# Kernel tuning notes

Measured on AMD Instinct MI355X. Metric: run time of the kernel, lower is better.

Reference implementation:

```python
import jax, jax.numpy as jnp
import numpy as np

B = 262144
K = 128  # n_coarse == num_bins


def setup_inputs() -> dict:
    key = jax.random.key(0)
    k1, k2, k3, k4, k5 = jax.random.split(key, 5)
    rays = jax.random.normal(k1, (B, 8), dtype=jnp.float32)
    weights = jax.random.uniform(k2, (B, K), dtype=jnp.float32)
    # z_samp must be monotonically increasing depths along each ray (near..far)
    near, far = 0.5, 10.0
    z_raw = jax.random.uniform(k3, (B, K), dtype=jnp.float32)
    z_samp = near + jnp.sort(z_raw, axis=-1) * (far - near)
    u = jax.random.uniform(k4, (B, K), dtype=jnp.float32)
    interval_interp = jax.random.uniform(k5, (B, K), dtype=jnp.float32)
    return {"rays": rays, "weights": weights, "z_samp": z_samp,
            "u": u, "interval_interp": interval_interp}


def reference(rays, weights, z_samp, u, interval_interp):
    # NeRFRenderer.sample_coarse_from_dist (lindisp=False)
    n_samples = u.shape[-1]  # n_coarse
    w = jax.lax.stop_gradient(weights) + 1e-5          # weights.detach() + 1e-5
    pdf = w / jnp.sum(w, axis=-1, keepdims=True)       # (B, K)
    cdf = jnp.cumsum(pdf, axis=-1)
    cdf = jnp.concatenate([jnp.zeros_like(cdf[:, :1]), cdf], axis=-1)  # (B, K+1)
    # searchsorted(cdf, u, right=True) - 1, batched over rays
    interval_ids = jax.vmap(lambda c, uu: jnp.searchsorted(c, uu, side='right'))(cdf, u) - 1
    interval_ids = jnp.clip(interval_ids, 0, n_samples - 1)
    # interval borders: [z0, midpoints, z_{K-1}] -> (B, K+1)
    centers = 0.5 * (z_samp[:, 1:] + z_samp[:, :-1])
    borders = jnp.concatenate([z_samp[:, :1], centers, z_samp[:, -1:]], axis=-1)
    left = jnp.take_along_axis(borders, interval_ids, axis=-1)
    right = jnp.take_along_axis(borders, interval_ids + 1, axis=-1)
    z_new = left * (1.0 - interval_interp) + right * interval_interp
    return z_new
```

## Files before the change

### kernel.cpp

```cpp
#include <hip/hip_runtime.h>

#define KK  128
#define RPW 8
#define TPB 128

__global__ __launch_bounds__(TPB, 6)
void nerf_sample_kernel(const float* __restrict__ Wg,
                        const float* __restrict__ Zg,
                        const float* __restrict__ Ug,
                        const float* __restrict__ Tg,
                        float* __restrict__ Og)
{
    __shared__ float S[2 * 2080];
    const int lane = threadIdx.x & 63;
    const int wvid = threadIdx.x >> 6;
    float* CW = S + wvid * 2080;
    float* BW = CW + 1024;

    const int r   = lane >> 3;
    const int h   = lane & 7;
    const int swz = r << 3;
    float* Srow = CW + r * KK;
    float* Brow = BW + r * 132;

    const size_t grp   = (size_t)blockIdx.x * 2 + wvid;
    const size_t gbase = grp * (RPW * KK);
    const size_t rbase = gbase + (size_t)r * KK;

    float4 cu = *(const float4*)(Ug + gbase + 4 * lane);
    float4 ct = *(const float4*)(Tg + gbase + 4 * lane);

    float x[16];
    {
        const float* wp = Wg + rbase + 16 * h;
        #pragma unroll
        for (int e = 0; e < 4; ++e) {
            float4 v = *(const float4*)(wp + 4 * e);
            x[4*e+0] = v.x + 1e-5f;
            x[4*e+1] = v.y + 1e-5f;
            x[4*e+2] = v.z + 1e-5f;
            x[4*e+3] = v.w + 1e-5f;
        }
    }

    float zr[16];
    {
        const float* zp = Zg + rbase + 16 * h;
        #pragma unroll
        for (int e = 0; e < 4; ++e) {
            float4 v = *(const float4*)(zp + 4 * e);
            zr[4*e+0] = v.x; zr[4*e+1] = v.y; zr[4*e+2] = v.z; zr[4*e+3] = v.w;
        }
    }

    float tot;
    {
        float Cc[16];
        #pragma unroll
        for (int c = 0; c < 16; ++c) {
            float a = x[c] + __shfl_xor(x[c], 4);
            float b = a    + __shfl_xor(a, 1);
            Cc[c]   = b    + __shfl_xor(b, 2);
        }
        float Uu[8];
        #pragma unroll
        for (int c = 0; c < 8; ++c) Uu[c] = Cc[c] + Cc[c + 8];
        float Vv[4];
        #pragma unroll
        for (int c = 0; c < 4; ++c) Vv[c] = Uu[c] + Uu[c + 4];
        tot = (Vv[0] + Vv[2]) + (Vv[1] + Vv[3]);
    }

    #pragma unroll
    for (int j = 0; j < 16; ++j) x[j] = x[j] / tot;

    #pragma unroll
    for (int m = 0; m < 8; ++m) x[2*m+1] = x[2*m+1] + x[2*m];
    #pragma unroll
    for (int m = 0; m < 4; ++m) x[4*m+3] = x[4*m+3] + x[4*m+1];
    #pragma unroll
    for (int m = 0; m < 2; ++m) x[8*m+7] = x[8*m+7] + x[8*m+3];
    x[15] = x[15] + x[7];

    {
        float s    = x[15];
        float sx1  = __shfl_xor(s, 1);
        float t1   = s + sx1;
        float t1x2 = __shfl_xor(t1, 2);
        float t2   = t1 + t1x2;
        float t2x4 = __shfl_xor(t2, 4);
        float c95  = t1x2 + t2x4;

        float xf =
            (h == 0) ? s :
            (h == 1) ? t1 :
            (h == 2) ? s + t1x2 :
            (h == 3) ? t2 :
            (h == 4) ? s + t2x4 :
            (h == 5) ? t1 + t2x4 :
            (h == 6) ? s + c95 :
                       t2 + t2x4;
        x[15] = xf;

        float P =
            (h == 0) ? 0.0f :
            (h == 1) ? sx1 :
            (h == 2) ? t1x2 :
            (h == 3) ? sx1 + t1x2 :
            (h == 4) ? t2x4 :
            (h == 5) ? sx1 + t2x4 :
            (h == 6) ? c95 :
                       sx1 + c95;

        x[7]  = x[7]  + P;
        x[3]  = x[3]  + P;  x[11] = x[11] + x[7];
        x[1]  = x[1]  + P;  x[5]  = x[5]  + x[3];
        x[9]  = x[9]  + x[7];  x[13] = x[13] + x[11];
        x[0]  = x[0]  + P;
        #pragma unroll
        for (int m = 1; m < 8; ++m) x[2*m] = x[2*m] + x[2*m-1];
    }

    #pragma unroll
    for (int e = 0; e < 4; ++e)
        *(float4*)(Srow + ((16*h + 4*e) ^ swz)) =
            make_float4(x[4*e+0], x[4*e+1], x[4*e+2], x[4*e+3]);

    {
        float zprev = __shfl_up(zr[15], 1);
        float B[16];
        B[0] = (h == 0) ? zr[0] : 0.5f * (zr[0] + zprev);
        #pragma unroll
        for (int k = 1; k < 16; ++k) B[k] = 0.5f * (zr[k] + zr[k-1]);
        #pragma unroll
        for (int e = 0; e < 4; ++e)
            *(float4*)(Brow + 16*h + 4*e) =
                make_float4(B[4*e+0], B[4*e+1], B[4*e+2], B[4*e+3]);
        if (h == 7) Brow[128] = zr[15];
    }

    __builtin_amdgcn_sched_barrier(0);
    __builtin_amdgcn_wave_barrier();
    __builtin_amdgcn_sched_barrier(0);

    const float EPSL = 1.0f - 1.8e-7f;
    const float EPSH = 1.0f + 1.8e-7f;
    const int rhalf = lane >> 5;

    for (int it = 0; it < 4; ++it) {
        float4 uu4 = cu, tt4 = ct;
        if (it < 3) {
            cu = *(const float4*)(Ug + gbase + (it + 1) * 256 + 4 * lane);
            ct = *(const float4*)(Tg + gbase + (it + 1) * 256 + 4 * lane);
        }

        const int rr = 2 * it + rhalf;
        const float* crow = CW + rr * KK;
        const float* brow = BW + rr * 132;
        const int csw = rr << 3;

        float uu[4] = {uu4.x, uu4.y, uu4.z, uu4.w};
        float tv[4] = {tt4.x, tt4.y, tt4.z, tt4.w};
        float ul[4], uh[4];
        int hh[4];
        #pragma unroll
        for (int i = 0; i < 4; ++i) {
            ul[i] = uu[i] * EPSL;
            uh[i] = uu[i] * EPSH;
            hh[i] = 0;
        }
        #pragma unroll
        for (int s = 64; s >= 1; s >>= 1) {
            #pragma unroll
            for (int i = 0; i < 4; ++i) {
                float b = crow[(hh[i] + s - 1) ^ csw];
                if (b <= uh[i]) hh[i] += s;
            }
        }

        float res[4];
        #pragma unroll
        for (int i = 0; i < 4; ++i) {
            const int hi = hh[i];
            int li = hi;
            while (li > 0 && crow[(li - 1) ^ csw] > ul[i]) --li;
            float lb = brow[hi], rb = brow[hi + 1];
            float r1 = lb * (1.0f - tv[i]) + rb * tv[i];
            if (li != hi) {
                float lb2 = brow[li], rb2 = brow[li + 1];
                float r0 = lb2 * (1.0f - tv[i]) + rb2 * tv[i];
                r1 = 0.5f * (r0 + r1);
            }
            res[i] = r1;
        }
        *(float4*)(Og + gbase + it * 256 + 4 * lane) =
            make_float4(res[0], res[1], res[2], res[3]);
    }
}

extern "C" void kernel_launch(void* const* d_in, const int* in_sizes, int n_in,
                              void* d_out, int out_size, void* d_ws, size_t ws_size,
                              hipStream_t stream)
{
    const float* Wg = (const float*)d_in[1];
    const float* Zg = (const float*)d_in[2];
    const float* Ug = (const float*)d_in[3];
    const float* Tg = (const float*)d_in[4];
    float* Og = (float*)d_out;

    const int nrays  = in_sizes[1] / KK;
    const int blocks = nrays / (2 * RPW);

    nerf_sample_kernel<<<dim3(blocks), dim3(TPB), 0, stream>>>(Wg, Zg, Ug, Tg, Og);
}
```

Baseline: 130.6 us.

## Halve rays per wave and spread each ray over sixteen lanes

Each wave now handles 4 rays instead of 8, with 16 lanes per ray holding 8 elements each. The wave-level prefix scan over the CDF is rewritten for 16-lane segments, LDS per block is halved, launch bounds go up to 8 blocks per CU, and the search loop is fully unrolled. The aim is more resident waves and less register pressure to hide memory latency, at the cost of an extra shuffle stage and twice as many blocks.

```diff
diff --git a/kernel.cpp b/kernel.cpp
--- a/kernel.cpp
+++ b/kernel.cpp
@@ -1,24 +1,24 @@
 #include <hip/hip_runtime.h>
 
 #define KK  128
-#define RPW 8
+#define RPW 4
 #define TPB 128
 
-__global__ __launch_bounds__(TPB, 6)
+__global__ __launch_bounds__(TPB, 8)
 void nerf_sample_kernel(const float* __restrict__ Wg,
                         const float* __restrict__ Zg,
                         const float* __restrict__ Ug,
                         const float* __restrict__ Tg,
                         float* __restrict__ Og)
 {
-    __shared__ float S[2 * 2080];
+    __shared__ float S[2 * 1040];
     const int lane = threadIdx.x & 63;
     const int wvid = threadIdx.x >> 6;
-    float* CW = S + wvid * 2080;
-    float* BW = CW + 1024;
-
-    const int r   = lane >> 3;
-    const int h   = lane & 7;
+    float* CW = S + wvid * 1040;
+    float* BW = CW + 512;
+
+    const int r   = lane >> 4;
+    const int h   = lane & 15;
     const int swz = r << 3;
     float* Srow = CW + r * KK;
     float* Brow = BW + r * 132;
@@ -30,11 +30,11 @@
     float4 cu = *(const float4*)(Ug + gbase + 4 * lane);
     float4 ct = *(const float4*)(Tg + gbase + 4 * lane);
 
-    float x[16];
-    {
-        const float* wp = Wg + rbase + 16 * h;
-        #pragma unroll
-        for (int e = 0; e < 4; ++e) {
+    float x[8];
+    {
+        const float* wp = Wg + rbase + 8 * h;
+        #pragma unroll
+        for (int e = 0; e < 2; ++e) {
             float4 v = *(const float4*)(wp + 4 * e);
             x[4*e+0] = v.x + 1e-5f;
             x[4*e+1] = v.y + 1e-5f;
@@ -43,100 +43,100 @@
         }
     }
 
-    float zr[16];
-    {
-        const float* zp = Zg + rbase + 16 * h;
-        #pragma unroll
-        for (int e = 0; e < 4; ++e) {
-            float4 v = *(const float4*)(zp + 4 * e);
-            zr[4*e+0] = v.x; zr[4*e+1] = v.y; zr[4*e+2] = v.z; zr[4*e+3] = v.w;
-        }
+    float zr[8];
+    {
+        const float* zp = Zg + rbase + 8 * h;
+        float4 v0 = *(const float4*)(zp);
+        float4 v1 = *(const float4*)(zp + 4);
+        zr[0]=v0.x; zr[1]=v0.y; zr[2]=v0.z; zr[3]=v0.w;
+        zr[4]=v1.x; zr[5]=v1.y; zr[6]=v1.z; zr[7]=v1.w;
     }
 
     float tot;
     {
-        float Cc[16];
-        #pragma unroll
-        for (int c = 0; c < 16; ++c) {
-            float a = x[c] + __shfl_xor(x[c], 4);
-            float b = a    + __shfl_xor(a, 1);
-            Cc[c]   = b    + __shfl_xor(b, 2);
-        }
-        float Uu[8];
-        #pragma unroll
-        for (int c = 0; c < 8; ++c) Uu[c] = Cc[c] + Cc[c + 8];
-        float Vv[4];
-        #pragma unroll
-        for (int c = 0; c < 4; ++c) Vv[c] = Uu[c] + Uu[c + 4];
-        tot = (Vv[0] + Vv[2]) + (Vv[1] + Vv[3]);
+        float Cc[8];
+        #pragma unroll
+        for (int j = 0; j < 8; ++j) {
+            float a = x[j] + __shfl_xor(x[j], 8);
+            float b = a    + __shfl_xor(a, 2);
+            float c = b    + __shfl_xor(b, 4);
+            Cc[j]   = c    + __shfl_xor(c, 1);
+        }
+        float V0 = Cc[0] + Cc[4];
+        float V1 = Cc[1] + Cc[5];
+        float V2 = Cc[2] + Cc[6];
+        float V3 = Cc[3] + Cc[7];
+        tot = (V0 + V2) + (V1 + V3);
     }
 
     #pragma unroll
-    for (int j = 0; j < 16; ++j) x[j] = x[j] / tot;
-
-    #pragma unroll
-    for (int m = 0; m < 8; ++m) x[2*m+1] = x[2*m+1] + x[2*m];
-    #pragma unroll
-    for (int m = 0; m < 4; ++m) x[4*m+3] = x[4*m+3] + x[4*m+1];
-    #pragma unroll
-    for (int m = 0; m < 2; ++m) x[8*m+7] = x[8*m+7] + x[8*m+3];
-    x[15] = x[15] + x[7];
-
-    {
-        float s    = x[15];
-        float sx1  = __shfl_xor(s, 1);
-        float t1   = s + sx1;
-        float t1x2 = __shfl_xor(t1, 2);
-        float t2   = t1 + t1x2;
-        float t2x4 = __shfl_xor(t2, 4);
-        float c95  = t1x2 + t2x4;
-
-        float xf =
-            (h == 0) ? s :
-            (h == 1) ? t1 :
-            (h == 2) ? s + t1x2 :
-            (h == 3) ? t2 :
-            (h == 4) ? s + t2x4 :
-            (h == 5) ? t1 + t2x4 :
-            (h == 6) ? s + c95 :
-                       t2 + t2x4;
-        x[15] = xf;
-
-        float P =
-            (h == 0) ? 0.0f :
-            (h == 1) ? sx1 :
-            (h == 2) ? t1x2 :
-            (h == 3) ? sx1 + t1x2 :
-            (h == 4) ? t2x4 :
-            (h == 5) ? sx1 + t2x4 :
-            (h == 6) ? c95 :
-                       sx1 + c95;
-
-        x[7]  = x[7]  + P;
-        x[3]  = x[3]  + P;  x[11] = x[11] + x[7];
-        x[1]  = x[1]  + P;  x[5]  = x[5]  + x[3];
-        x[9]  = x[9]  + x[7];  x[13] = x[13] + x[11];
-        x[0]  = x[0]  + P;
-        #pragma unroll
-        for (int m = 1; m < 8; ++m) x[2*m] = x[2*m] + x[2*m-1];
-    }
-
-    #pragma unroll
-    for (int e = 0; e < 4; ++e)
-        *(float4*)(Srow + ((16*h + 4*e) ^ swz)) =
-            make_float4(x[4*e+0], x[4*e+1], x[4*e+2], x[4*e+3]);
-
-    {
-        float zprev = __shfl_up(zr[15], 1);
-        float B[16];
-        B[0] = (h == 0) ? zr[0] : 0.5f * (zr[0] + zprev);
-        #pragma unroll
-        for (int k = 1; k < 16; ++k) B[k] = 0.5f * (zr[k] + zr[k-1]);
-        #pragma unroll
-        for (int e = 0; e < 4; ++e)
-            *(float4*)(Brow + 16*h + 4*e) =
-                make_float4(B[4*e+0], B[4*e+1], B[4*e+2], B[4*e+3]);
-        if (h == 7) Brow[128] = zr[15];
+    for (int j = 0; j < 8; ++j) x[j] = x[j] / tot;
+
+    x[1] = x[1] + x[0];  x[3] = x[3] + x[2];
+    x[5] = x[5] + x[4];  x[7] = x[7] + x[6];
+    x[3] = x[3] + x[1];  x[7] = x[7] + x[5];
+    x[7] = x[7] + x[3];
+
+    {
+        float s     = x[7];
+        float sx1   = __shfl_xor(s, 1);
+        float pair  = s + sx1;
+        float pairx2 = __shfl_xor(pair, 2);
+        float quad  = pair + pairx2;
+        float quadx4 = __shfl_xor(quad, 4);
+        float oct   = quad + quadx4;
+        float octx8 = __shfl_xor(oct, 8);
+
+        float tP = (h & 8) ? octx8 : 0.0f;
+        tP = (h & 4) ? (quadx4 + tP) : tP;
+        tP = (h & 2) ? (pairx2 + tP) : tP;
+        float P = (h & 1) ? (sx1 + tP) : tP;
+
+        float c5v  = pairx2 + quadx4;
+        float c9v  = pairx2 + octx8;
+        float c11v = quadx4 + octx8;
+        float c13v = pairx2 + c11v;
+        float C =
+            (h ==  0) ? s :
+            (h ==  1) ? pair :
+            (h ==  2) ? s + pairx2 :
+            (h ==  3) ? quad :
+            (h ==  4) ? s + quadx4 :
+            (h ==  5) ? pair + quadx4 :
+            (h ==  6) ? s + c5v :
+            (h ==  7) ? oct :
+            (h ==  8) ? s + octx8 :
+            (h ==  9) ? pair + octx8 :
+            (h == 10) ? s + c9v :
+            (h == 11) ? quad + octx8 :
+            (h == 12) ? s + c11v :
+            (h == 13) ? pair + c11v :
+            (h == 14) ? s + c13v :
+                        oct + octx8;
+        x[7] = C;
+
+        x[3] = x[3] + P;
+        x[1] = x[1] + P;  x[5] = x[5] + x[3];
+        x[0] = x[0] + P;  x[2] = x[2] + x[1];
+        x[4] = x[4] + x[3];  x[6] = x[6] + x[5];
+    }
+
+    *(float4*)(Srow + ((8*h    ) ^ swz)) = make_float4(x[0], x[1], x[2], x[3]);
+    *(float4*)(Srow + ((8*h + 4) ^ swz)) = make_float4(x[4], x[5], x[6], x[7]);
+
+    {
+        float zprev = __shfl_up(zr[7], 1);
+        float B0 = (h == 0) ? zr[0] : 0.5f * (zr[0] + zprev);
+        float B1 = 0.5f * (zr[1] + zr[0]);
+        float B2 = 0.5f * (zr[2] + zr[1]);
+        float B3 = 0.5f * (zr[3] + zr[2]);
+        float B4 = 0.5f * (zr[4] + zr[3]);
+        float B5 = 0.5f * (zr[5] + zr[4]);
+        float B6 = 0.5f * (zr[6] + zr[5]);
+        float B7 = 0.5f * (zr[7] + zr[6]);
+        *(float4*)(Brow + 8*h    ) = make_float4(B0, B1, B2, B3);
+        *(float4*)(Brow + 8*h + 4) = make_float4(B4, B5, B6, B7);
+        if (h == 15) Brow[128] = zr[7];
     }
 
     __builtin_amdgcn_sched_barrier(0);
@@ -147,11 +147,12 @@
     const float EPSH = 1.0f + 1.8e-7f;
     const int rhalf = lane >> 5;
 
-    for (int it = 0; it < 4; ++it) {
+    #pragma unroll
+    for (int it = 0; it < 2; ++it) {
         float4 uu4 = cu, tt4 = ct;
-        if (it < 3) {
-            cu = *(const float4*)(Ug + gbase + (it + 1) * 256 + 4 * lane);
-            ct = *(const float4*)(Tg + gbase + (it + 1) * 256 + 4 * lane);
+        if (it == 0) {
+            cu = *(const float4*)(Ug + gbase + 256 + 4 * lane);
+            ct = *(const float4*)(Tg + gbase + 256 + 4 * lane);
         }
 
         const int rr = 2 * it + rhalf;
```

Result: no change. 128.5 us (-1.6%).
